# Performance work log

Hardware: AMD Instinct MI355X
Metric: run time of the kernel (lower is better)

Reference implementation:

```python
import jax, jax.numpy as jnp
from jax import lax
import numpy as np

B, CIN, COUT = 8, 16, 32
HA = WA = HB = WB = 24
GROUPS = 4
EPS = 1e-5


def _conv2d(x, w, b):
    # x: (N, Cin, H, W), w: (Cout, Cin, kh, kw), stride 1, padding 1
    y = lax.conv_general_dilated(x, w, window_strides=(1, 1),
                                 padding=[(1, 1), (1, 1)],
                                 dimension_numbers=('NCHW', 'OIHW', 'NCHW'))
    return y + b[None, :, None, None]


def _group_norm(x, gamma, beta):
    # x: (B, C, ha, wa, hb, wb); normalize per sample within channel groups
    b, c = x.shape[0], x.shape[1]
    xg = x.reshape(b, GROUPS, c // GROUPS, *x.shape[2:])
    mean = jnp.mean(xg, axis=tuple(range(2, xg.ndim)), keepdims=True)
    var = jnp.var(xg, axis=tuple(range(2, xg.ndim)), keepdims=True)
    xn = ((xg - mean) * lax.rsqrt(var + EPS)).reshape(x.shape)
    shape = (1, c) + (1,) * (x.ndim - 2)
    return xn * gamma.reshape(shape) + beta.reshape(shape)


def setup_inputs() -> dict:
    key = jax.random.key(0)
    ks = jax.random.split(key, 5)
    return {
        'x': jax.random.normal(ks[0], (B, CIN, HA, WA, HB, WB), dtype=jnp.float32),
        'conv1_w': jax.random.normal(ks[1], (COUT, COUT, 3, 3), dtype=jnp.float32) * 0.05,
        'conv1_b': jax.random.normal(ks[2], (COUT,), dtype=jnp.float32) * 0.01,
        'conv2_w': jax.random.normal(ks[3], (COUT, CIN, 3, 3), dtype=jnp.float32) * 0.05,
        'conv2_b': jax.random.normal(ks[4], (COUT,), dtype=jnp.float32) * 0.01,
        'gn2_gamma': jnp.ones((COUT,), dtype=jnp.float32),
        'gn2_beta': jnp.zeros((COUT,), dtype=jnp.float32),
    }


def reference(x, conv1_w, conv1_b, conv2_w, conv2_b, gn2_gamma, gn2_beta):
    bsz, inch, ha, wa, hb, wb = x.shape
    # conv over (hb, wb) plane: fold (b, ha, wa) into batch
    out = x.transpose(0, 2, 3, 1, 4, 5).reshape(bsz * ha * wa, inch, hb, wb)
    out = _conv2d(out, conv2_w, conv2_b)
    outch, o_hb, o_wb = out.shape[-3:]
    out = out.reshape(bsz, ha, wa, outch, o_hb, o_wb).transpose(0, 3, 1, 2, 4, 5)
    out = _group_norm(out, gn2_gamma, gn2_beta)
    out = jax.nn.relu(out)
    # conv over (ha, wa) plane: fold (b, hb, wb) into batch
    out = out.transpose(0, 4, 5, 1, 2, 3).reshape(bsz * o_hb * o_wb, outch, ha, wa)
    out = _conv2d(out, conv1_w, conv1_b)
    outch, o_ha, o_wa = out.shape[-3:]
    out = out.reshape(bsz, o_hb, o_wb, outch, o_ha, o_wa).transpose(0, 3, 4, 5, 1, 2)
    return out
```

## Files before the change

### kernel.cpp

```cpp
#include <hip/hip_runtime.h>

constexpr int BN   = 8;
constexpr int CIN  = 16;
constexpr int COUT = 32;
constexpr int S    = 24;
constexpr int P    = S * S;
constexpr int SP   = 26;
constexpr int PPAD = SP * SP;
constexpr int NPIX = P * P;
constexpr int NREP = 8;
constexpr float EPS = 1e-5f;

__device__ __forceinline__ void barrier_lgkm() {
    asm volatile("s_waitcnt lgkmcnt(0)" ::: "memory");
    __builtin_amdgcn_s_barrier();
    asm volatile("" ::: "memory");
}

__global__ void zero_stats_kernel(float* __restrict__ stats) {
    stats[threadIdx.x] = 0.f;
    stats[threadIdx.x + 256] = 0.f;
}

__global__ __launch_bounds__(256, 3)
void conv2_kernel(const float* __restrict__ x, const float* __restrict__ w2,
                  const float* __restrict__ b2, float* __restrict__ inter,
                  float* __restrict__ stats)
{
    __shared__ float xs[PPAD];

    const int tid = threadIdx.x;
    const int bid = blockIdx.x;
    const int b   = bid & 7;
    const int haw = bid >> 3;

    for (int i = tid; i < PPAD; i += 256) xs[i] = 0.f;

    const int wave = tid >> 6, lane = tid & 63;
    const int co0 = wave * 8;
    const int co0u = __builtin_amdgcn_readfirstlane(co0);

    const float4 bA = *(const float4*)(b2 + co0);
    const float4 bB = *(const float4*)(b2 + co0 + 4);
    float4 accA[9], accB[9];
    int base[9];
#pragma unroll
    for (int j = 0; j < 9; ++j) {
        accA[j] = bA; accB[j] = bB;
        const int p = lane + 64 * j;
        const int hb = p / 24, wb = p - hb * 24;
        base[j] = hb * SP + wb;
    }

    const bool act = tid < 144;
    int xoff = 0;
    if (act) {
        const int hb = tid / 6, wb0 = 4 * (tid % 6);
        xoff = (hb + 1) * SP + (wb0 + 1);
    }
    const float* xb0 = x + ((size_t)(b * CIN) * P + haw) * P;
    float4 stg = make_float4(0.f, 0.f, 0.f, 0.f);
    if (act) stg = *(const float4*)(xb0 + 4 * tid);

    barrier_lgkm();

#pragma unroll 1
    for (int ci = 0; ci < CIN; ++ci) {
        if (act) *(float4*)(xs + xoff) = stg;
        if (ci + 1 < CIN && act)
            stg = *(const float4*)(xb0 + (size_t)(ci + 1) * NPIX + 4 * tid);
        barrier_lgkm();
        const float* wci = w2 + (size_t)co0u * (CIN * 9) + ci * 9;
#pragma unroll
        for (int tap = 0; tap < 9; ++tap) {
            const int off = (tap / 3) * SP + (tap % 3);
            const float wk0 = wci[0 * 144 + tap];
            const float wk1 = wci[1 * 144 + tap];
            const float wk2 = wci[2 * 144 + tap];
            const float wk3 = wci[3 * 144 + tap];
            const float wk4 = wci[4 * 144 + tap];
            const float wk5 = wci[5 * 144 + tap];
            const float wk6 = wci[6 * 144 + tap];
            const float wk7 = wci[7 * 144 + tap];
#pragma unroll
            for (int j = 0; j < 9; ++j) {
                const float v = xs[base[j] + off];
                accA[j].x = fmaf(v, wk0, accA[j].x);
                accA[j].y = fmaf(v, wk1, accA[j].y);
                accA[j].z = fmaf(v, wk2, accA[j].z);
                accA[j].w = fmaf(v, wk3, accA[j].w);
                accB[j].x = fmaf(v, wk4, accB[j].x);
                accB[j].y = fmaf(v, wk5, accB[j].y);
                accB[j].z = fmaf(v, wk6, accB[j].z);
                accB[j].w = fmaf(v, wk7, accB[j].w);
            }
        }
        barrier_lgkm();
    }

    float s = 0.f, ss = 0.f;
    float* dst = inter + (size_t)((b * COUT + co0) * P + haw) * P;
#pragma unroll
    for (int j = 0; j < 9; ++j) {
        const int p = lane + 64 * j;
        const float4 a = accA[j], c = accB[j];
        s  += a.x + a.y + a.z + a.w + c.x + c.y + c.z + c.w;
        ss += a.x*a.x + a.y*a.y + a.z*a.z + a.w*a.w
            + c.x*c.x + c.y*c.y + c.z*c.z + c.w*c.w;
        dst[0 * NPIX + p] = a.x; dst[1 * NPIX + p] = a.y;
        dst[2 * NPIX + p] = a.z; dst[3 * NPIX + p] = a.w;
        dst[4 * NPIX + p] = c.x; dst[5 * NPIX + p] = c.y;
        dst[6 * NPIX + p] = c.z; dst[7 * NPIX + p] = c.w;
    }
#pragma unroll
    for (int off = 32; off > 0; off >>= 1) {
        s  += __shfl_down(s, off);
        ss += __shfl_down(ss, off);
    }
    if (lane == 0) {
        float* st = stats + ((unsigned)haw & (NREP - 1)) * 64;
        atomicAdd(&st[(b * 4 + wave) * 2 + 0], s);
        atomicAdd(&st[(b * 4 + wave) * 2 + 1], ss);
    }
}

__global__ void gn_finalize_kernel(const float* __restrict__ stats,
                                   const float* __restrict__ gamma,
                                   const float* __restrict__ beta,
                                   float* __restrict__ scale,
                                   float* __restrict__ shift)
{
    const int t = threadIdx.x;
    const int b = t >> 5, c = t & 31, g = c >> 3;
    float sum = 0.f, ssq = 0.f;
#pragma unroll
    for (int r = 0; r < NREP; ++r) {
        sum += stats[r * 64 + (b * 4 + g) * 2 + 0];
        ssq += stats[r * 64 + (b * 4 + g) * 2 + 1];
    }
    const float invN = 1.f / (8.f * (float)NPIX);
    const float mean = sum * invN;
    const float var  = ssq * invN - mean * mean;
    const float rstd = rsqrtf(var + EPS);
    const float sc   = gamma[c] * rstd;
    scale[t] = sc;
    shift[t] = beta[c] - mean * sc;
}

__global__ __launch_bounds__(256, 3)
void conv1_kernel(const float* __restrict__ inter, const float* __restrict__ w1,
                  const float* __restrict__ b1, const float* __restrict__ scale,
                  const float* __restrict__ shift, float* __restrict__ out)
{
    __shared__ float pl[9 * P];
    __shared__ float scs[COUT], shs[COUT];

    const int tid = threadIdx.x;
    const int bid = blockIdx.x;
    const int b   = bid & 7;
    const int haw = bid >> 3;
    const int ha  = haw / 24, wa = haw - ha * 24;

    for (int i = tid; i < 9 * P; i += 256) pl[i] = 0.f;
    if (tid < COUT) {
        scs[tid] = scale[b * 32 + tid];
        shs[tid] = shift[b * 32 + tid];
    }

    const int wave = tid >> 6, lane = tid & 63;
    const int co0 = wave * 8;
    const int co0u = __builtin_amdgcn_readfirstlane(co0);

    int off[6];
#pragma unroll
    for (int k = 0; k < 6; ++k) {
        const int c = tid + 256 * k;
        off[k] = -1;
        if (c < 1296) {
            const int q = c / 144, r = c - q * 144;
            const int ha2 = ha + q / 3 - 1, wa2 = wa + (q % 3) - 1;
            if (((unsigned)ha2 < 24u) && ((unsigned)wa2 < 24u))
                off[k] = (ha2 * 24 + wa2) * P + 4 * r;
        }
    }

    const float* ib0 = inter + (size_t)(b * COUT) * NPIX;
    float4 stg[6];
#pragma unroll
    for (int k = 0; k < 6; ++k) {
        stg[k] = make_float4(0.f, 0.f, 0.f, 0.f);
        if (off[k] >= 0) stg[k] = *(const float4*)(ib0 + off[k]);
    }

    const float4 bA = *(const float4*)(b1 + co0);
    const float4 bB = *(const float4*)(b1 + co0 + 4);
    float4 accA[9], accB[9];
#pragma unroll
    for (int j = 0; j < 9; ++j) { accA[j] = bA; accB[j] = bB; }

    barrier_lgkm();

#pragma unroll 1
    for (int ci = 0; ci < COUT; ++ci) {
        const float sc = scs[ci], sh = shs[ci];
#pragma unroll
        for (int k = 0; k < 6; ++k) {
            if (off[k] >= 0) {
                const float4 v = stg[k];
                float4 w;
                w.x = fmaxf(fmaf(v.x, sc, sh), 0.f);
                w.y = fmaxf(fmaf(v.y, sc, sh), 0.f);
                w.z = fmaxf(fmaf(v.z, sc, sh), 0.f);
                w.w = fmaxf(fmaf(v.w, sc, sh), 0.f);
                *(float4*)(pl + 4 * (tid + 256 * k)) = w;
            }
        }
        if (ci + 1 < COUT) {
            const float* ib = ib0 + (size_t)(ci + 1) * NPIX;
#pragma unroll
            for (int k = 0; k < 6; ++k)
                if (off[k] >= 0) stg[k] = *(const float4*)(ib + off[k]);
        }
        barrier_lgkm();
        const float* wci = w1 + (size_t)co0u * (COUT * 9) + ci * 9;
#pragma unroll
        for (int tap = 0; tap < 9; ++tap) {
            const float wk0 = wci[0 * 288 + tap];
            const float wk1 = wci[1 * 288 + tap];
            const float wk2 = wci[2 * 288 + tap];
            const float wk3 = wci[3 * 288 + tap];
            const float wk4 = wci[4 * 288 + tap];
            const float wk5 = wci[5 * 288 + tap];
            const float wk6 = wci[6 * 288 + tap];
            const float wk7 = wci[7 * 288 + tap];
#pragma unroll
            for (int j = 0; j < 9; ++j) {
                const float v = pl[tap * P + lane + 64 * j];
                accA[j].x = fmaf(v, wk0, accA[j].x);
                accA[j].y = fmaf(v, wk1, accA[j].y);
                accA[j].z = fmaf(v, wk2, accA[j].z);
                accA[j].w = fmaf(v, wk3, accA[j].w);
                accB[j].x = fmaf(v, wk4, accB[j].x);
                accB[j].y = fmaf(v, wk5, accB[j].y);
                accB[j].z = fmaf(v, wk6, accB[j].z);
                accB[j].w = fmaf(v, wk7, accB[j].w);
            }
        }
        barrier_lgkm();
    }

    float* dst = out + (size_t)((b * COUT + co0) * P + haw) * P;
#pragma unroll
    for (int j = 0; j < 9; ++j) {
        const int p = lane + 64 * j;
        dst[0 * NPIX + p] = accA[j].x; dst[1 * NPIX + p] = accA[j].y;
        dst[2 * NPIX + p] = accA[j].z; dst[3 * NPIX + p] = accA[j].w;
        dst[4 * NPIX + p] = accB[j].x; dst[5 * NPIX + p] = accB[j].y;
        dst[6 * NPIX + p] = accB[j].z; dst[7 * NPIX + p] = accB[j].w;
    }
}

extern "C" void kernel_launch(void* const* d_in, const int* in_sizes, int n_in,
                              void* d_out, int out_size, void* d_ws, size_t ws_size,
                              hipStream_t stream) {
    const float* x       = (const float*)d_in[0];
    const float* conv1_w = (const float*)d_in[1];
    const float* conv1_b = (const float*)d_in[2];
    const float* conv2_w = (const float*)d_in[3];
    const float* conv2_b = (const float*)d_in[4];
    const float* gamma   = (const float*)d_in[5];
    const float* beta    = (const float*)d_in[6];
    float* out = (float*)d_out;

    float* wsf   = (float*)d_ws;
    float* stats = wsf;
    float* scale = wsf + 512;
    float* shift = wsf + 768;
    float* inter = wsf + 1024;

    zero_stats_kernel<<<1, 256, 0, stream>>>(stats);
    conv2_kernel<<<BN * P, 256, 0, stream>>>(x, conv2_w, conv2_b, inter, stats);
    gn_finalize_kernel<<<1, 256, 0, stream>>>(stats, gamma, beta, scale, shift);
    conv1_kernel<<<BN * P, 256, 0, stream>>>(inter, conv1_w, conv1_b,
                                             scale, shift, out);
}
```

Baseline: 1.271 ms.

## Stage all input channels in LDS upfront and process conv taps row-wise

conv2_kernel now loads all 16 input-channel planes into a CIN x 26x26 shared buffer in one go, with 9 float4 loads per thread in flight. This removes the per-channel barriers and the serialized single-plane staging. The inner loop now walks kernel rows, loading 24 weights and three neighbouring LDS values per row. LDS use grows from about 2.7KB to about 43KB per block, which with launch_bounds(256,3) may limit occupancy, and the larger weight arrays raise register pressure.

```diff
diff --git a/kernel.cpp b/kernel.cpp
--- a/kernel.cpp
+++ b/kernel.cpp
@@ -27,18 +27,35 @@
                   const float* __restrict__ b2, float* __restrict__ inter,
                   float* __restrict__ stats)
 {
-    __shared__ float xs[PPAD];
+    __shared__ float xs[CIN][PPAD];
 
     const int tid = threadIdx.x;
     const int bid = blockIdx.x;
     const int b   = bid & 7;
     const int haw = bid >> 3;
 
-    for (int i = tid; i < PPAD; i += 256) xs[i] = 0.f;
-
     const int wave = tid >> 6, lane = tid & 63;
     const int co0 = wave * 8;
     const int co0u = __builtin_amdgcn_readfirstlane(co0);
+
+    const float* xb0 = x + ((size_t)(b * CIN) * P + haw) * P;
+    float4 stg[9];
+    int wo[9];
+#pragma unroll
+    for (int k = 0; k < 9; ++k) {
+        const int c  = tid + 256 * k;
+        const int ci = c / 144, r = c - ci * 144;
+        stg[k] = *(const float4*)(xb0 + (size_t)ci * NPIX + 4 * r);
+        const int hb = r / 6, wb0 = 4 * (r % 6);
+        wo[k] = ci * PPAD + (hb + 1) * SP + (wb0 + 1);
+    }
+
+    for (int i = tid; i < CIN * PPAD; i += 256) (&xs[0][0])[i] = 0.f;
+    barrier_lgkm();
+#pragma unroll
+    for (int k = 0; k < 9; ++k)
+        *(float4*)(&xs[0][0] + wo[k]) = stg[k];
+    barrier_lgkm();
 
     const float4 bA = *(const float4*)(b2 + co0);
     const float4 bB = *(const float4*)(b2 + co0 + 4);
@@ -52,50 +69,36 @@
         base[j] = hb * SP + wb;
     }
 
-    const bool act = tid < 144;
-    int xoff = 0;
-    if (act) {
-        const int hb = tid / 6, wb0 = 4 * (tid % 6);
-        xoff = (hb + 1) * SP + (wb0 + 1);
-    }
-    const float* xb0 = x + ((size_t)(b * CIN) * P + haw) * P;
-    float4 stg = make_float4(0.f, 0.f, 0.f, 0.f);
-    if (act) stg = *(const float4*)(xb0 + 4 * tid);
-
-    barrier_lgkm();
-
 #pragma unroll 1
     for (int ci = 0; ci < CIN; ++ci) {
-        if (act) *(float4*)(xs + xoff) = stg;
-        if (ci + 1 < CIN && act)
-            stg = *(const float4*)(xb0 + (size_t)(ci + 1) * NPIX + 4 * tid);
-        barrier_lgkm();
+        const float* xci = &xs[ci][0];
         const float* wci = w2 + (size_t)co0u * (CIN * 9) + ci * 9;
 #pragma unroll
-        for (int tap = 0; tap < 9; ++tap) {
-            const int off = (tap / 3) * SP + (tap % 3);
-            const float wk0 = wci[0 * 144 + tap];
-            const float wk1 = wci[1 * 144 + tap];
-            const float wk2 = wci[2 * 144 + tap];
-            const float wk3 = wci[3 * 144 + tap];
-            const float wk4 = wci[4 * 144 + tap];
-            const float wk5 = wci[5 * 144 + tap];
-            const float wk6 = wci[6 * 144 + tap];
-            const float wk7 = wci[7 * 144 + tap];
+        for (int kh = 0; kh < 3; ++kh) {
+            const float* wr = wci + kh * 3;
+            float wk[8][3];
+#pragma unroll
+            for (int m = 0; m < 8; ++m) {
+                wk[m][0] = wr[m * 144 + 0];
+                wk[m][1] = wr[m * 144 + 1];
+                wk[m][2] = wr[m * 144 + 2];
+            }
 #pragma unroll
             for (int j = 0; j < 9; ++j) {
-                const float v = xs[base[j] + off];
-                accA[j].x = fmaf(v, wk0, accA[j].x);
-                accA[j].y = fmaf(v, wk1, accA[j].y);
-                accA[j].z = fmaf(v, wk2, accA[j].z);
-                accA[j].w = fmaf(v, wk3, accA[j].w);
-                accB[j].x = fmaf(v, wk4, accB[j].x);
-                accB[j].y = fmaf(v, wk5, accB[j].y);
-                accB[j].z = fmaf(v, wk6, accB[j].z);
-                accB[j].w = fmaf(v, wk7, accB[j].w);
-            }
-        }
-        barrier_lgkm();
+                const float* xr = xci + base[j] + kh * SP;
+                const float v0 = xr[0];
+                const float v1 = xr[1];
+                const float v2 = xr[2];
+                accA[j].x = fmaf(v0, wk[0][0], fmaf(v1, wk[0][1], fmaf(v2, wk[0][2], accA[j].x)));
+                accA[j].y = fmaf(v0, wk[1][0], fmaf(v1, wk[1][1], fmaf(v2, wk[1][2], accA[j].y)));
+                accA[j].z = fmaf(v0, wk[2][0], fmaf(v1, wk[2][1], fmaf(v2, wk[2][2], accA[j].z)));
+                accA[j].w = fmaf(v0, wk[3][0], fmaf(v1, wk[3][1], fmaf(v2, wk[3][2], accA[j].w)));
+                accB[j].x = fmaf(v0, wk[4][0], fmaf(v1, wk[4][1], fmaf(v2, wk[4][2], accB[j].x)));
+                accB[j].y = fmaf(v0, wk[5][0], fmaf(v1, wk[5][1], fmaf(v2, wk[5][2], accB[j].y)));
+                accB[j].z = fmaf(v0, wk[6][0], fmaf(v1, wk[6][1], fmaf(v2, wk[6][2], accB[j].z)));
+                accB[j].w = fmaf(v0, wk[7][0], fmaf(v1, wk[7][1], fmaf(v2, wk[7][2], accB[j].w)));
+            }
+        }
     }
 
     float s = 0.f, ss = 0.f;
```

New measurement: 1.265 ms. No clear change (-0.5%).
